# Kernel optimization log

Hardware: AMD Instinct MI355X
Metric: run time of the kernel (lower is better)

Reference implementation:

```python
import jax, jax.numpy as jnp
import numpy as np

B, N, HID, H = 16, 256, 512, 8
DK = HID // H          # att_size = 64
FEAT = 8               # storage/operator feature dim
MLP_H = 64             # interaction MLP hidden dim
LAM = 0.1              # htap_lambda
SCALE = DK ** -0.5


def _pair_bias(feat, W1, b1, W2, b2):
    """MLP([v_i || v_j || |v_i - v_j|]) for all pairs -> [B,N,N,H].
    Split W1 over the three concat blocks so the per-node parts are O(N)."""
    F = feat.shape[-1]
    Wa, Wb, Wc = W1[:F], W1[F:2 * F], W1[2 * F:]
    hi = feat @ Wa                                    # [B,N,MLP_H]
    hj = feat @ Wb                                    # [B,N,MLP_H]
    diff = jnp.abs(feat[:, :, None, :] - feat[:, None, :, :])  # [B,N,N,F]
    h = jax.nn.relu(hi[:, :, None, :] + hj[:, None, :, :] + diff @ Wc + b1)
    return h @ W2 + b2                                # [B,N,N,H]


def setup_inputs() -> dict:
    key = jax.random.key(0)
    ks = jax.random.split(key, 24)
    g = lambda i, shape, s=0.05: jax.random.normal(ks[i], shape, jnp.float32) * (1.0 if s is None else 1.0) * (s / 0.05 * 0.05 if False else 1.0)
    def w(i, shape, scale):
        return jax.random.normal(ks[i], shape, jnp.float32) * scale
    inp = {
        "q": w(0, (B, N, HID), 1.0),
        "k": w(1, (B, N, HID), 1.0),
        "v": w(2, (B, N, HID), 1.0),
        "tree_attn_bias": w(3, (B, H, N, N), 1.0),
        "storage_features": w(4, (B, N, FEAT), 1.0),
        "operator_features": w(5, (B, N, FEAT), 1.0),
        # attention projections (stored as [in,out])
        "Wq": w(6, (HID, HID), HID ** -0.5), "bq": jnp.zeros((HID,), jnp.float32),
        "Wk": w(7, (HID, HID), HID ** -0.5), "bk": jnp.zeros((HID,), jnp.float32),
        "Wv": w(8, (HID, HID), HID ** -0.5), "bv": jnp.zeros((HID,), jnp.float32),
        "Wo": w(9, (HID, HID), HID ** -0.5), "bo": jnp.zeros((HID,), jnp.float32),
        # f_s interaction MLP: Linear(3*FEAT,64) -> ReLU -> Linear(64,H)
        "fs_W1": w(10, (3 * FEAT, MLP_H), (3 * FEAT) ** -0.5), "fs_b1": jnp.zeros((MLP_H,), jnp.float32),
        "fs_W2": w(11, (MLP_H, H), MLP_H ** -0.5), "fs_b2": jnp.zeros((H,), jnp.float32),
        # f_o interaction MLP
        "fo_W1": w(12, (3 * FEAT, MLP_H), (3 * FEAT) ** -0.5), "fo_b1": jnp.zeros((MLP_H,), jnp.float32),
        "fo_W2": w(13, (MLP_H, H), MLP_H ** -0.5), "fo_b2": jnp.zeros((H,), jnp.float32),
    }
    return inp


def reference(q, k, v, tree_attn_bias, storage_features, operator_features,
              Wq, bq, Wk, bk, Wv, bv, Wo, bo,
              fs_W1, fs_b1, fs_W2, fs_b2, fo_W1, fo_b1, fo_W2, fo_b2):
    # projections -> [B,H,N,DK]
    qh = (q @ Wq + bq).reshape(B, N, H, DK).transpose(0, 2, 1, 3) * SCALE
    kh = (k @ Wk + bk).reshape(B, N, H, DK).transpose(0, 2, 1, 3)
    vh = (v @ Wv + bv).reshape(B, N, H, DK).transpose(0, 2, 1, 3)

    scores = jnp.einsum("bhnd,bhmd->bhnm", qh, kh) + tree_attn_bias

    htap = (_pair_bias(storage_features, fs_W1, fs_b1, fs_W2, fs_b2)
            + _pair_bias(operator_features, fo_W1, fo_b1, fo_W2, fo_b2))  # [B,N,N,H]
    scores = scores + LAM * htap.transpose(0, 3, 1, 2)

    attn = jax.nn.softmax(scores, axis=-1)            # dropout rate 0 (eval)
    x = jnp.einsum("bhnm,bhmd->bhnd", attn, vh)
    x = x.transpose(0, 2, 1, 3).reshape(B, N, HID)
    return x @ Wo + bo
```

## Files before the change

kernel.cpp:

```cpp
#include <hip/hip_runtime.h>
#include <hip/hip_bf16.h>
#include <stdint.h>

#define B_    16
#define N_    256
#define HID_  512
#define H_    8
#define DK_   64
#define FEAT_ 8
#define MLPH_ 64
#define LAM_  0.1f
#define SCALE_ 0.125f

typedef short bf16x8 __attribute__((ext_vector_type(8)));
typedef float f32x4  __attribute__((ext_vector_type(4)));

union U8 { uint4 u; bf16x8 h; ushort s[8]; };

__device__ __forceinline__ uint16_t f32_to_bf16(float x) {
    uint32_t u = __float_as_uint(x);
    u += 0x7fffu + ((u >> 16) & 1u);
    return (uint16_t)(u >> 16);
}
__device__ __forceinline__ float bf16_to_f32(uint16_t v) {
    return __uint_as_float(((uint32_t)v) << 16);
}
__device__ __forceinline__ uint32_t pk_bf16(float lo, float hi) {
    float2 xy; xy.x = lo; xy.y = hi;
    __hip_bfloat162 b2 = __float22bfloat162_rn(xy);
    return *(uint32_t*)&b2;
}
#define LDS_FENCE() asm volatile("s_waitcnt lgkmcnt(0)" ::: "memory")

__global__ __launch_bounds__(256, 4) void proj_kernel(
    const float* __restrict__ q, const float* __restrict__ k, const float* __restrict__ v,
    const float* __restrict__ Wq, const float* __restrict__ bq,
    const float* __restrict__ Wk, const float* __restrict__ bk,
    const float* __restrict__ Wv, const float* __restrict__ bv,
    ushort* __restrict__ qh, ushort* __restrict__ kh, ushort* __restrict__ vh)
{
    int z = blockIdx.z;
    const float* X    = (z == 0) ? q  : (z == 1) ? k  : v;
    const float* W    = (z == 0) ? Wq : (z == 1) ? Wk : Wv;
    const float* bias = (z == 0) ? bq : (z == 1) ? bk : bv;
    ushort* out       = (z == 0) ? qh : (z == 1) ? kh : vh;
    float scale       = (z == 0) ? SCALE_ : 1.0f;

    int m0 = blockIdx.x * 64;
    int h  = blockIdx.y;
    int c0 = h * 64;

    __shared__ __align__(16) ushort Xs[2][64 * 40];
    __shared__ __align__(16) ushort Ws[2][64 * 40];

    int t = threadIdx.x;
    int wave = t >> 6, lane = t & 63;
    int l15 = lane & 15, qd = lane >> 4;

    int xr = t >> 2, xc = (t & 3) * 8;
    int kr = t & 15, nq = t >> 4;

    f32x4 acc[4] = {};

    float4 xa, xb, w0, w1;
    xa = *(const float4*)&X[(m0 + xr) * HID_ + xc];
    xb = *(const float4*)&X[(m0 + xr) * HID_ + xc + 4];
    w0 = *(const float4*)&W[(2 * kr) * HID_ + c0 + nq * 4];
    w1 = *(const float4*)&W[(2 * kr + 1) * HID_ + c0 + nq * 4];

    for (int k0 = 0; k0 < HID_; k0 += 32) {
        int buf = (k0 >> 5) & 1;
        {
            uint4 o;
            o.x = (uint32_t)f32_to_bf16(xa.x) | ((uint32_t)f32_to_bf16(xa.y) << 16);
            o.y = (uint32_t)f32_to_bf16(xa.z) | ((uint32_t)f32_to_bf16(xa.w) << 16);
            o.z = (uint32_t)f32_to_bf16(xb.x) | ((uint32_t)f32_to_bf16(xb.y) << 16);
            o.w = (uint32_t)f32_to_bf16(xb.z) | ((uint32_t)f32_to_bf16(xb.w) << 16);
            *(uint4*)&Xs[buf][xr * 40 + xc] = o;
        }
        {
            const float* a0 = &w0.x; const float* a1 = &w1.x;
            #pragma unroll
            for (int i = 0; i < 4; i++) {
                uint32_t pk = (uint32_t)f32_to_bf16(a0[i]) | ((uint32_t)f32_to_bf16(a1[i]) << 16);
                *(uint32_t*)&Ws[buf][(nq * 4 + i) * 40 + 2 * kr] = pk;
            }
        }
        __syncthreads();

        if (k0 + 32 < HID_) {
            int kn = k0 + 32;
            xa = *(const float4*)&X[(m0 + xr) * HID_ + kn + xc];
            xb = *(const float4*)&X[(m0 + xr) * HID_ + kn + xc + 4];
            w0 = *(const float4*)&W[(kn + 2 * kr) * HID_ + c0 + nq * 4];
            w1 = *(const float4*)&W[(kn + 2 * kr + 1) * HID_ + c0 + nq * 4];
        }

        bf16x8 af = *(const bf16x8*)&Xs[buf][(wave * 16 + l15) * 40 + qd * 8];
        #pragma unroll
        for (int nt = 0; nt < 4; nt++) {
            bf16x8 bf = *(const bf16x8*)&Ws[buf][(nt * 16 + l15) * 40 + qd * 8];
            acc[nt] = __builtin_amdgcn_mfma_f32_16x16x32_bf16(af, bf, acc[nt], 0, 0, 0);
        }
    }

    #pragma unroll
    for (int nt = 0; nt < 4; nt++) {
        float bb = bias[c0 + nt * 16 + l15];
        #pragma unroll
        for (int r = 0; r < 4; r++) {
            int m = m0 + wave * 16 + qd * 4 + r;
            int b_ = m >> 8, n_ = m & 255;
            float val = (acc[nt][r] + bb) * scale;
            out[(((b_ * H_ + h) * N_) + n_) * DK_ + nt * 16 + l15] = f32_to_bf16(val);
        }
    }
}

__global__ void prep_frags(const float* __restrict__ fsW1, const float* __restrict__ foW1,
                           const float* __restrict__ fsW2, const float* __restrict__ foW2,
                           uint4* __restrict__ bfrag1, uint4* __restrict__ bfrag2)
{
    int t = threadIdx.x;
    #pragma unroll
    for (int e = t; e < 512; e += 256) {
        int nt = e >> 6, lane = e & 63, l15 = lane & 15, qd = lane >> 4;
        int n = nt * 16 + l15;
        ushort vals[8];
        #pragma unroll
        for (int u = 0; u < 8; u++) {
            float x = 0.f;
            if (n < 64) {
                if (qd == 0) x = fsW1[(16 + u) * 64 + n];
                else if (qd == 1) x = fsW1[(8 + u) * 64 + n];
            } else {
                int n2 = n - 64;
                if (qd == 2) x = foW1[(16 + u) * 64 + n2];
                else if (qd == 3) x = foW1[(8 + u) * 64 + n2];
            }
            vals[u] = f32_to_bf16(x);
        }
        uint4 pk;
        pk.x = (uint32_t)vals[0] | ((uint32_t)vals[1] << 16);
        pk.y = (uint32_t)vals[2] | ((uint32_t)vals[3] << 16);
        pk.z = (uint32_t)vals[4] | ((uint32_t)vals[5] << 16);
        pk.w = (uint32_t)vals[6] | ((uint32_t)vals[7] << 16);
        bfrag1[e] = pk;
    }
    {
        int e = t;
        int ks = e >> 6, lane = e & 63, l15 = lane & 15, qd = lane >> 4;
        ushort vals[8];
        #pragma unroll
        for (int u = 0; u < 8; u++) {
            float x = 0.f;
            if (l15 < 8) {
                int k2 = ks * 32 + qd * 8 + u;
                int c = ((k2 & 7) << 4) | (k2 >> 3);
                x = LAM_ * ((c < 64) ? fsW2[c * 8 + l15] : foW2[(c - 64) * 8 + l15]);
            }
            vals[u] = f32_to_bf16(x);
        }
        uint4 pk;
        pk.x = (uint32_t)vals[0] | ((uint32_t)vals[1] << 16);
        pk.y = (uint32_t)vals[2] | ((uint32_t)vals[3] << 16);
        pk.z = (uint32_t)vals[4] | ((uint32_t)vals[5] << 16);
        pk.w = (uint32_t)vals[6] | ((uint32_t)vals[7] << 16);
        bfrag2[e] = pk;
    }
}

#define HSTRIDE 136
__global__ __launch_bounds__(256, 3) void pair_bias_mfma(
    const float* __restrict__ sf, const float* __restrict__ of,
    const float* __restrict__ fsW1, const float* __restrict__ fsb1,
    const float* __restrict__ foW1, const float* __restrict__ fob1,
    const float* __restrict__ fsb2, const float* __restrict__ fob2,
    const uint4* __restrict__ bfrag1, const uint4* __restrict__ bfrag2,
    ushort* __restrict__ mlpb)
{
    __shared__ __align__(16) ushort hbuf[4][2][16 * HSTRIDE];
    __shared__ float hisbuf[128];
    __shared__ __align__(4) ushort tbuf[4][2][8 * 16];

    int i = blockIdx.x, b = blockIdx.y;
    int t = threadIdx.x;
    int wave = t >> 6, lane = t & 63;
    int l15 = lane & 15, qd = lane >> 4;

    if (t < 128) {
        int set = t >> 6, kk = t & 63;
        const float* W1 = set ? foW1 : fsW1;
        const float* fi = (set ? of : sf) + (b * N_ + i) * FEAT_;
        float a = (set ? fob1 : fsb1)[kk];
        #pragma unroll
        for (int f = 0; f < FEAT_; f++) a += fi[f] * W1[f * 64 + kk];
        hisbuf[t] = a;
    }

    bf16x8 Bf1[8], Bf2[4];
    #pragma unroll
    for (int nt = 0; nt < 8; nt++) { U8 u; u.u = bfrag1[nt * 64 + lane]; Bf1[nt] = u.h; }
    #pragma unroll
    for (int ks = 0; ks < 4; ks++) { U8 u; u.u = bfrag2[ks * 64 + lane]; Bf2[ks] = u.h; }

    const float* fsr = sf + (b * N_ + i) * FEAT_;
    const float* forr = of + (b * N_ + i) * FEAT_;
    float fsi[8], foi[8];
    #pragma unroll
    for (int u = 0; u < 8; u++) { fsi[u] = fsr[u]; foi[u] = forr[u]; }
    float b2l = LAM_ * (fsb2[l15 & 7] + fob2[l15 & 7]);

    bf16x8 af[4];
    #pragma unroll
    for (int qt = 0; qt < 4; qt++) {
        int j = (wave * 4 + qt) * 16 + l15;
        const float* fr = ((qd < 2) ? sf : of) + (b * N_ + j) * FEAT_;
        float4 f0 = *(const float4*)&fr[0];
        float4 f1 = *(const float4*)&fr[4];
        float vals[8] = {f0.x, f0.y, f0.z, f0.w, f1.x, f1.y, f1.z, f1.w};
        if ((qd & 1) == 0) {
            const float* fi = (qd < 2) ? fsi : foi;
            #pragma unroll
            for (int u = 0; u < 8; u++) vals[u] = fabsf(vals[u] - fi[u]);
        }
        U8 au;
        #pragma unroll
        for (int p = 0; p < 4; p++)
            ((uint32_t*)&au)[p] = pk_bf16(vals[2 * p], vals[2 * p + 1]);
        af[qt] = au.h;
    }

    __syncthreads();
    float hv[8];
    #pragma unroll
    for (int nt = 0; nt < 8; nt++) hv[nt] = hisbuf[nt * 16 + l15];

    {
        f32x4 S1[8];
        #pragma unroll
        for (int nt = 0; nt < 8; nt++) {
            f32x4 c0 = {hv[nt], hv[nt], hv[nt], hv[nt]};
            S1[nt] = __builtin_amdgcn_mfma_f32_16x16x32_bf16(af[0], Bf1[nt], c0, 0, 0, 0);
        }
        ushort* hb = &hbuf[wave][0][0];
        #pragma unroll
        for (int r = 0; r < 4; r++) {
            uint4 w;
            w.x = pk_bf16(fmaxf(S1[0][r], 0.f), fmaxf(S1[1][r], 0.f));
            w.y = pk_bf16(fmaxf(S1[2][r], 0.f), fmaxf(S1[3][r], 0.f));
            w.z = pk_bf16(fmaxf(S1[4][r], 0.f), fmaxf(S1[5][r], 0.f));
            w.w = pk_bf16(fmaxf(S1[6][r], 0.f), fmaxf(S1[7][r], 0.f));
            *(uint4*)&hb[(qd * 4 + r) * HSTRIDE + l15 * 8] = w;
        }
    }

    #pragma unroll
    for (int qt = 0; qt < 4; qt++) {
        ushort* hbC = &hbuf[wave][qt & 1][0];
        ushort* hbN = &hbuf[wave][(qt & 1) ^ 1][0];
        LDS_FENCE();

        f32x4 Sn[8];
        if (qt < 3) {
            #pragma unroll
            for (int nt = 0; nt < 8; nt++) {
                f32x4 c0 = {hv[nt], hv[nt], hv[nt], hv[nt]};
                Sn[nt] = __builtin_amdgcn_mfma_f32_16x16x32_bf16(af[qt + 1], Bf1[nt], c0, 0, 0, 0);
            }
        }

        f32x4 S2 = {b2l, b2l, b2l, b2l};
        #pragma unroll
        for (int ks = 0; ks < 4; ks++) {
            bf16x8 a2 = *(const bf16x8*)&hbC[l15 * HSTRIDE + ks * 32 + qd * 8];
            S2 = __builtin_amdgcn_mfma_f32_16x16x32_bf16(a2, Bf2[ks], S2, 0, 0, 0);
        }

        ushort* tb = &tbuf[wave][qt & 1][0];
        if (l15 < 8) {
            #pragma unroll
            for (int r = 0; r < 4; r++)
                tb[l15 * 16 + qd * 4 + r] = f32_to_bf16(S2[r]);
        }
        LDS_FENCE();

        {
            int j0 = (wave * 4 + qt) * 16;
            int h2 = lane >> 3, jp = lane & 7;
            uint32_t lo = tb[h2 * 16 + jp * 2];
            uint32_t hi = tb[h2 * 16 + jp * 2 + 1];
            uint32_t pk = lo | (hi << 16);
            *(uint32_t*)&mlpb[(((size_t)(b * H_ + h2) * N_ + i) * N_) + j0 + jp * 2] = pk;
        }

        if (qt < 3) {
            #pragma unroll
            for (int r = 0; r < 4; r++) {
                uint4 w;
                w.x = pk_bf16(fmaxf(Sn[0][r], 0.f), fmaxf(Sn[1][r], 0.f));
                w.y = pk_bf16(fmaxf(Sn[2][r], 0.f), fmaxf(Sn[3][r], 0.f));
                w.z = pk_bf16(fmaxf(Sn[4][r], 0.f), fmaxf(Sn[5][r], 0.f));
                w.w = pk_bf16(fmaxf(Sn[6][r], 0.f), fmaxf(Sn[7][r], 0.f));
                *(uint4*)&hbN[(qd * 4 + r) * HSTRIDE + l15 * 8] = w;
            }
        }
    }
}

__global__ __launch_bounds__(256, 2) void attn_kernel(
    const ushort* __restrict__ qh, const ushort* __restrict__ kh,
    const ushort* __restrict__ vh, const float* __restrict__ tree,
    const ushort* __restrict__ mlpb, ushort* __restrict__ ctxb)
{
    __shared__ __align__(16) ushort bufKP[256 * 72];
    __shared__ __align__(16) ushort bufV[64 * 264];

    int blk = blockIdx.x;
    int bh = blk >> 2;
    int quarter = blk & 3;

    int t = threadIdx.x;
    int wave = t >> 6, lane = t & 63;
    int l15 = lane & 15, qd = lane >> 4;
    int i0w = quarter * 64 + wave * 16;

    const ushort* khb = kh + (size_t)bh * N_ * DK_;
    const ushort* vhb = vh + (size_t)bh * N_ * DK_;

    #pragma unroll
    for (int u = t; u < 2048; u += 256) {
        int j = u >> 3, seg = (u & 7) * 8;
        uint4 kv = *(const uint4*)&khb[j * DK_ + seg];
        *(uint4*)&bufKP[j * 72 + seg] = kv;
    }
    #pragma unroll
    for (int u = t; u < 1024; u += 256) {
        int rp = u & 127, d0 = (u >> 7) * 8;
        U8 v0, v1;
        v0.u = *(const uint4*)&vhb[(2 * rp) * DK_ + d0];
        v1.u = *(const uint4*)&vhb[(2 * rp + 1) * DK_ + d0];
        #pragma unroll
        for (int jj = 0; jj < 8; jj++) {
            uint32_t pk = (uint32_t)v0.s[jj] | ((uint32_t)v1.s[jj] << 16);
            *(uint32_t*)&bufV[(d0 + jj) * 264 + 2 * rp] = pk;
        }
    }
    __syncthreads();

    bf16x8 a0, a1;
    {
        size_t qb = ((size_t)bh * N_ + i0w + l15) * DK_;
        U8 t0, t1;
        t0.u = *(const uint4*)&qh[qb + qd * 8];
        t1.u = *(const uint4*)&qh[qb + 32 + qd * 8];
        a0 = t0.h; a1 = t1.h;
    }
    f32x4 S[16];
    #pragma unroll
    for (int nt = 0; nt < 16; nt++) {
        f32x4 acc = {};
        bf16x8 b0 = *(const bf16x8*)&bufKP[(nt * 16 + l15) * 72 + qd * 8];
        bf16x8 b1 = *(const bf16x8*)&bufKP[(nt * 16 + l15) * 72 + 32 + qd * 8];
        acc = __builtin_amdgcn_mfma_f32_16x16x32_bf16(a0, b0, acc, 0, 0, 0);
        acc = __builtin_amdgcn_mfma_f32_16x16x32_bf16(a1, b1, acc, 0, 0, 0);
        S[nt] = acc;
    }

    {
        size_t base = ((size_t)bh * N_ + i0w + qd * 4) * N_ + l15;
        const float*  tr = tree + base;
        const ushort* mb = mlpb + base;
        #pragma unroll
        for (int nt = 0; nt < 16; nt++)
            #pragma unroll
            for (int r = 0; r < 4; r++)
                S[nt][r] += tr[(size_t)r * N_ + nt * 16] + bf16_to_f32(mb[(size_t)r * N_ + nt * 16]);
    }

    float mx[4], sm[4];
    #pragma unroll
    for (int r = 0; r < 4; r++) mx[r] = -1e30f;
    #pragma unroll
    for (int nt = 0; nt < 16; nt++)
        #pragma unroll
        for (int r = 0; r < 4; r++) mx[r] = fmaxf(mx[r], S[nt][r]);
    #pragma unroll
    for (int r = 0; r < 4; r++) {
        #pragma unroll
        for (int m = 1; m <= 8; m <<= 1) mx[r] = fmaxf(mx[r], __shfl_xor(mx[r], m));
    }
    #pragma unroll
    for (int r = 0; r < 4; r++) sm[r] = 0.f;
    #pragma unroll
    for (int nt = 0; nt < 16; nt++)
        #pragma unroll
        for (int r = 0; r < 4; r++) {
            float e = __expf(S[nt][r] - mx[r]);
            S[nt][r] = e;
            sm[r] += e;
        }
    #pragma unroll
    for (int r = 0; r < 4; r++) {
        #pragma unroll
        for (int m = 1; m <= 8; m <<= 1) sm[r] += __shfl_xor(sm[r], m);
        sm[r] = 1.0f / sm[r];
    }

    __syncthreads();

    {
        uint32_t* Pw = (uint32_t*)&bufKP[wave * 16 * 264];
        #pragma unroll
        for (int nt = 0; nt < 16; nt++)
            #pragma unroll
            for (int r = 0; r < 4; r++) {
                float p = S[nt][r] * sm[r];
                float po = __shfl_xor(p, 1);
                uint32_t pk = (uint32_t)f32_to_bf16(p) | ((uint32_t)f32_to_bf16(po) << 16);
                if ((lane & 1) == 0)
                    Pw[(qd * 4 + r) * 132 + nt * 8 + (l15 >> 1)] = pk;
            }
    }
    __syncthreads();

    const ushort* Pw = &bufKP[wave * 16 * 264];
    f32x4 O[4] = {};
    #pragma unroll
    for (int ks = 0; ks < 8; ks++) {
        int j0 = ks * 32;
        bf16x8 pa = *(const bf16x8*)&Pw[l15 * 264 + j0 + qd * 8];
        #pragma unroll
        for (int ntd = 0; ntd < 4; ntd++) {
            bf16x8 vb = *(const bf16x8*)&bufV[(ntd * 16 + l15) * 264 + j0 + qd * 8];
            O[ntd] = __builtin_amdgcn_mfma_f32_16x16x32_bf16(pa, vb, O[ntd], 0, 0, 0);
        }
    }

    #pragma unroll
    for (int ntd = 0; ntd < 4; ntd++)
        #pragma unroll
        for (int r = 0; r < 4; r++)
            ctxb[((size_t)bh * N_ + i0w + qd * 4 + r) * DK_ + ntd * 16 + l15] =
                f32_to_bf16(O[ntd][r]);
}

__global__ __launch_bounds__(256, 4) void outproj_kernel(
    const ushort* __restrict__ ctxb, const float* __restrict__ Wo,
    const float* __restrict__ bo, float* __restrict__ out)
{
    int m0 = blockIdx.x * 64;
    int c0 = blockIdx.y * 64;

    __shared__ __align__(16) ushort Xs[64 * 40];
    __shared__ __align__(16) ushort Ws[64 * 40];

    int t = threadIdx.x;
    int wave = t >> 6, lane = t & 63;
    int l15 = lane & 15, qd = lane >> 4;

    f32x4 acc[4] = {};

    for (int k0 = 0; k0 < HID_; k0 += 32) {
        __syncthreads();
        {
            int r = t >> 2, s8 = (t & 3) * 8;
            int m = m0 + r, b_ = m >> 8, n_ = m & 255;
            uint4 xv = *(const uint4*)&ctxb[(((b_ * H_ + (k0 >> 6)) * N_) + n_) * DK_ + (k0 & 63) + s8];
            *(uint4*)&Xs[r * 40 + s8] = xv;
        }
        {
            int kr = t & 15, nq = t >> 4;
            float4 w0 = *(const float4*)&Wo[(k0 + 2 * kr) * HID_ + c0 + nq * 4];
            float4 w1 = *(const float4*)&Wo[(k0 + 2 * kr + 1) * HID_ + c0 + nq * 4];
            const float* a0 = &w0.x; const float* a1 = &w1.x;
            #pragma unroll
            for (int i = 0; i < 4; i++) {
                uint32_t pk = (uint32_t)f32_to_bf16(a0[i]) | ((uint32_t)f32_to_bf16(a1[i]) << 16);
                *(uint32_t*)&Ws[(nq * 4 + i) * 40 + 2 * kr] = pk;
            }
        }
        __syncthreads();
        bf16x8 af = *(const bf16x8*)&Xs[(wave * 16 + l15) * 40 + qd * 8];
        #pragma unroll
        for (int nt = 0; nt < 4; nt++) {
            bf16x8 bf = *(const bf16x8*)&Ws[(nt * 16 + l15) * 40 + qd * 8];
            acc[nt] = __builtin_amdgcn_mfma_f32_16x16x32_bf16(af, bf, acc[nt], 0, 0, 0);
        }
    }

    #pragma unroll
    for (int nt = 0; nt < 4; nt++) {
        float bb = bo[c0 + nt * 16 + l15];
        #pragma unroll
        for (int r = 0; r < 4; r++) {
            int m = m0 + wave * 16 + qd * 4 + r;
            out[m * HID_ + c0 + nt * 16 + l15] = acc[nt][r] + bb;
        }
    }
}

extern "C" void kernel_launch(void* const* d_in, const int* in_sizes, int n_in,
                              void* d_out, int out_size, void* d_ws, size_t ws_size,
                              hipStream_t stream)
{
    const float* q    = (const float*)d_in[0];
    const float* k    = (const float*)d_in[1];
    const float* v    = (const float*)d_in[2];
    const float* tree = (const float*)d_in[3];
    const float* sf   = (const float*)d_in[4];
    const float* of   = (const float*)d_in[5];
    const float* Wq   = (const float*)d_in[6];
    const float* bq   = (const float*)d_in[7];
    const float* Wk   = (const float*)d_in[8];
    const float* bk   = (const float*)d_in[9];
    const float* Wv   = (const float*)d_in[10];
    const float* bv   = (const float*)d_in[11];
    const float* Wo   = (const float*)d_in[12];
    const float* bo   = (const float*)d_in[13];
    const float* fsW1 = (const float*)d_in[14];
    const float* fsb1 = (const float*)d_in[15];
    const float* fsW2 = (const float*)d_in[16];
    const float* fsb2 = (const float*)d_in[17];
    const float* foW1 = (const float*)d_in[18];
    const float* fob1 = (const float*)d_in[19];
    const float* foW2 = (const float*)d_in[20];
    const float* fob2 = (const float*)d_in[21];

    char* ws = (char*)d_ws;
    ushort* qh     = (ushort*)(ws + 0);
    ushort* kh     = (ushort*)(ws + 4194304);
    ushort* vh     = (ushort*)(ws + 8388608);
    ushort* ctxb   = (ushort*)(ws + 12582912);
    uint4*  bfrag1 = (uint4*)(ws + 16777216);
    uint4*  bfrag2 = (uint4*)(ws + 16785408);
    ushort* mlpb   = (ushort*)(ws + 23080960);

    proj_kernel<<<dim3(64, 8, 3), 256, 0, stream>>>(q, k, v, Wq, bq, Wk, bk, Wv, bv, qh, kh, vh);
    prep_frags<<<1, 256, 0, stream>>>(fsW1, foW1, fsW2, foW2, bfrag1, bfrag2);
    pair_bias_mfma<<<dim3(N_, B_), 256, 0, stream>>>(sf, of, fsW1, fsb1, foW1, fob1,
                                                     fsb2, fob2, bfrag1, bfrag2, mlpb);
    attn_kernel<<<512, 256, 0, stream>>>(qh, kh, vh, tree, mlpb, ctxb);
    outproj_kernel<<<dim3(64, 8), 256, 0, stream>>>(ctxb, Wo, bo, (float*)d_out);
}
```

Baseline: 231.3 us.

## Restructure projection GEMM into two big K-halves with register-held X fragments

The projection kernel drops the per-32-column double-buffered LDS loop. It now loads half of K (256) of W into a swizzled LDS tile in one step, and each lane loads its X MFMA fragments straight from global memory into registers, with no X staging in LDS. The aim is to cut the number of barriers and loop iterations and to issue more global loads at once for memory-level parallelism. In exchange, register and LDS use rise sharply (32KB LDS, 16 float4 plus 16 bf16x8 live), so launch bounds drop to 2 blocks per SM and occupancy falls.

```diff
diff --git a/kernel.cpp b/kernel.cpp
--- a/kernel.cpp
+++ b/kernel.cpp
@@ -32,7 +32,7 @@
 }
 #define LDS_FENCE() asm volatile("s_waitcnt lgkmcnt(0)" ::: "memory")
 
-__global__ __launch_bounds__(256, 4) void proj_kernel(
+__global__ __launch_bounds__(256, 2) void proj_kernel(
     const float* __restrict__ q, const float* __restrict__ k, const float* __restrict__ v,
     const float* __restrict__ Wq, const float* __restrict__ bq,
     const float* __restrict__ Wk, const float* __restrict__ bk,
@@ -50,57 +50,102 @@
     int h  = blockIdx.y;
     int c0 = h * 64;
 
-    __shared__ __align__(16) ushort Xs[2][64 * 40];
-    __shared__ __align__(16) ushort Ws[2][64 * 40];
+    __shared__ __align__(16) ushort Ws[16384];
 
     int t = threadIdx.x;
     int wave = t >> 6, lane = t & 63;
     int l15 = lane & 15, qd = lane >> 4;
 
-    int xr = t >> 2, xc = (t & 3) * 8;
     int kr = t & 15, nq = t >> 4;
+    int slotw = kr >> 2, elemw = (2 * kr) & 7;
+
+    int xrow = m0 + wave * 16 + l15;
+    const float* Xr = X + (size_t)xrow * HID_;
 
     f32x4 acc[4] = {};
 
-    float4 xa, xb, w0, w1;
-    xa = *(const float4*)&X[(m0 + xr) * HID_ + xc];
-    xb = *(const float4*)&X[(m0 + xr) * HID_ + xc + 4];
-    w0 = *(const float4*)&W[(2 * kr) * HID_ + c0 + nq * 4];
-    w1 = *(const float4*)&W[(2 * kr + 1) * HID_ + c0 + nq * 4];
-
-    for (int k0 = 0; k0 < HID_; k0 += 32) {
-        int buf = (k0 >> 5) & 1;
-        {
-            uint4 o;
-            o.x = (uint32_t)f32_to_bf16(xa.x) | ((uint32_t)f32_to_bf16(xa.y) << 16);
-            o.y = (uint32_t)f32_to_bf16(xa.z) | ((uint32_t)f32_to_bf16(xa.w) << 16);
-            o.z = (uint32_t)f32_to_bf16(xb.x) | ((uint32_t)f32_to_bf16(xb.y) << 16);
-            o.w = (uint32_t)f32_to_bf16(xb.z) | ((uint32_t)f32_to_bf16(xb.w) << 16);
-            *(uint4*)&Xs[buf][xr * 40 + xc] = o;
-        }
-        {
-            const float* a0 = &w0.x; const float* a1 = &w1.x;
-            #pragma unroll
-            for (int i = 0; i < 4; i++) {
-                uint32_t pk = (uint32_t)f32_to_bf16(a0[i]) | ((uint32_t)f32_to_bf16(a1[i]) << 16);
-                *(uint32_t*)&Ws[buf][(nq * 4 + i) * 40 + 2 * kr] = pk;
-            }
-        }
-        __syncthreads();
-
-        if (k0 + 32 < HID_) {
-            int kn = k0 + 32;
-            xa = *(const float4*)&X[(m0 + xr) * HID_ + kn + xc];
-            xb = *(const float4*)&X[(m0 + xr) * HID_ + kn + xc + 4];
-            w0 = *(const float4*)&W[(kn + 2 * kr) * HID_ + c0 + nq * 4];
-            w1 = *(const float4*)&W[(kn + 2 * kr + 1) * HID_ + c0 + nq * 4];
-        }
-
-        bf16x8 af = *(const bf16x8*)&Xs[buf][(wave * 16 + l15) * 40 + qd * 8];
+    float4 wv[16];
+    #pragma unroll
+    for (int c = 0; c < 8; c++) {
+        wv[2 * c]     = *(const float4*)&W[(c * 32 + 2 * kr) * HID_ + c0 + nq * 4];
+        wv[2 * c + 1] = *(const float4*)&W[(c * 32 + 2 * kr + 1) * HID_ + c0 + nq * 4];
+    }
+    bf16x8 xf[8];
+    #pragma unroll
+    for (int c = 0; c < 8; c++) {
+        float4 xa = *(const float4*)&Xr[c * 32 + qd * 8];
+        float4 xb = *(const float4*)&Xr[c * 32 + qd * 8 + 4];
+        U8 u;
+        ((uint32_t*)&u)[0] = pk_bf16(xa.x, xa.y);
+        ((uint32_t*)&u)[1] = pk_bf16(xa.z, xa.w);
+        ((uint32_t*)&u)[2] = pk_bf16(xb.x, xb.y);
+        ((uint32_t*)&u)[3] = pk_bf16(xb.z, xb.w);
+        xf[c] = u.h;
+    }
+    #pragma unroll
+    for (int c = 0; c < 8; c++) {
+        const float* a0 = &wv[2 * c].x;
+        const float* a1 = &wv[2 * c + 1].x;
+        #pragma unroll
+        for (int i = 0; i < 4; i++) {
+            int n = nq * 4 + i;
+            int idx = c * 2048 + n * 32 + ((slotw ^ ((n >> 1) & 3)) * 8) + elemw;
+            *(uint32_t*)&Ws[idx] =
+                (uint32_t)f32_to_bf16(a0[i]) | ((uint32_t)f32_to_bf16(a1[i]) << 16);
+        }
+    }
+    __syncthreads();
+
+    #pragma unroll
+    for (int c = 0; c < 8; c++) {
+        wv[2 * c]     = *(const float4*)&W[(256 + c * 32 + 2 * kr) * HID_ + c0 + nq * 4];
+        wv[2 * c + 1] = *(const float4*)&W[(256 + c * 32 + 2 * kr + 1) * HID_ + c0 + nq * 4];
+    }
+    bf16x8 xg[8];
+    #pragma unroll
+    for (int c = 0; c < 8; c++) {
+        float4 xa = *(const float4*)&Xr[256 + c * 32 + qd * 8];
+        float4 xb = *(const float4*)&Xr[256 + c * 32 + qd * 8 + 4];
+        U8 u;
+        ((uint32_t*)&u)[0] = pk_bf16(xa.x, xa.y);
+        ((uint32_t*)&u)[1] = pk_bf16(xa.z, xa.w);
+        ((uint32_t*)&u)[2] = pk_bf16(xb.x, xb.y);
+        ((uint32_t*)&u)[3] = pk_bf16(xb.z, xb.w);
+        xg[c] = u.h;
+    }
+
+    #pragma unroll
+    for (int c = 0; c < 8; c++) {
         #pragma unroll
         for (int nt = 0; nt < 4; nt++) {
-            bf16x8 bf = *(const bf16x8*)&Ws[buf][(nt * 16 + l15) * 40 + qd * 8];
-            acc[nt] = __builtin_amdgcn_mfma_f32_16x16x32_bf16(af, bf, acc[nt], 0, 0, 0);
+            int n = nt * 16 + l15;
+            bf16x8 bf = *(const bf16x8*)&Ws[c * 2048 + n * 32 + ((qd ^ ((n >> 1) & 3)) * 8)];
+            acc[nt] = __builtin_amdgcn_mfma_f32_16x16x32_bf16(xf[c], bf, acc[nt], 0, 0, 0);
+        }
+    }
+    __syncthreads();
+
+    #pragma unroll
+    for (int c = 0; c < 8; c++) {
+        const float* a0 = &wv[2 * c].x;
+        const float* a1 = &wv[2 * c + 1].x;
+        #pragma unroll
+        for (int i = 0; i < 4; i++) {
+            int n = nq * 4 + i;
+            int idx = c * 2048 + n * 32 + ((slotw ^ ((n >> 1) & 3)) * 8) + elemw;
+            *(uint32_t*)&Ws[idx] =
+                (uint32_t)f32_to_bf16(a0[i]) | ((uint32_t)f32_to_bf16(a1[i]) << 16);
+        }
+    }
+    __syncthreads();
+
+    #pragma unroll
+    for (int c = 0; c < 8; c++) {
+        #pragma unroll
+        for (int nt = 0; nt < 4; nt++) {
+            int n = nt * 16 + l15;
+            bf16x8 bf = *(const bf16x8*)&Ws[c * 2048 + n * 32 + ((qd ^ ((n >> 1) & 3)) * 8)];
+            acc[nt] = __builtin_amdgcn_mfma_f32_16x16x32_bf16(xg[c], bf, acc[nt], 0, 0, 0);
         }
     }
 
```

After: 238.8 us. 1.03x slower.
